# Kernel tuning notes

Measured on AMD Instinct MI355X. Metric: run time of the kernel, lower is better.

## Reference

```python
import jax, jax.numpy as jnp
import numpy as np

B, S, D = 2, 2048, 2048
H = 16
HD = D // H            # 128 head dim
L = 512                # latent dim
R = 64                 # rope dim (min(64, HD) = 64)
RH = R // 2
SCALE = HD ** -0.5     # note: uses head_dim, not head_dim+rope_dim
NEG = jnp.float32(-1e9)


def _rope_tables():
    inv_freq = 1.0 / (10000.0 ** (jnp.arange(0, R, 2, dtype=jnp.float32) / R))  # [RH]
    pos = jnp.arange(S, dtype=jnp.float32)
    freqs = pos[:, None] * inv_freq[None, :]  # [S, RH]
    return jnp.cos(freqs), jnp.sin(freqs)


def _apply_rope(x, cos, sin):
    # x: [B, H, S, R], interleaved even/odd rotation as in the torch source
    xe, xo = x[..., 0::2], x[..., 1::2]                    # [B,H,S,RH]
    c = cos[None, None]
    s = sin[None, None]
    re = xe * c - xo * s
    ro = xe * s + xo * c
    return jnp.stack([re, ro], axis=-1).reshape(x.shape)   # re-interleave


def setup_inputs() -> dict:
    key = jax.random.key(0)
    ks = jax.random.split(key, 8)
    std = 0.02
    f32 = jnp.float32
    return {
        "x":     jax.random.normal(ks[0], (B, S, D), f32),
        "W_ckv": jax.random.normal(ks[1], (D, L), f32) * std,      # compress_kv
        "W_kv":  jax.random.normal(ks[2], (L, 2 * D), f32) * std,  # kv_proj
        "W_cq":  jax.random.normal(ks[3], (D, L), f32) * std,      # compress_q
        "W_q":   jax.random.normal(ks[4], (L, D), f32) * std,      # q_proj
        "W_qr":  jax.random.normal(ks[5], (L, H * R), f32) * std,  # q_rope
        "W_kr":  jax.random.normal(ks[6], (L, R), f32) * std,      # k_rope
        "W_out": jax.random.normal(ks[7], (D, D), f32) * std,      # out_proj
    }


def reference(x, W_ckv, W_kv, W_cq, W_q, W_qr, W_kr, W_out):
    cos, sin = _rope_tables()

    c_kv = x @ W_ckv                                   # [B,S,L]
    kv = c_kv @ W_kv                                   # [B,S,2D]
    c_q = x @ W_cq                                     # [B,S,L]

    q_c = (c_q @ W_q).reshape(B, S, H, HD).transpose(0, 2, 1, 3)    # [B,H,S,HD]
    q_r = (c_q @ W_qr).reshape(B, S, H, R).transpose(0, 2, 1, 3)    # [B,H,S,R]
    k_r = (c_kv @ W_kr)[:, None, :, :]                               # [B,1,S,R]

    k_c, v = jnp.split(kv, 2, axis=-1)
    k_c = k_c.reshape(B, S, H, HD).transpose(0, 2, 1, 3)             # [B,H,S,HD]
    v = v.reshape(B, S, H, HD).transpose(0, 2, 1, 3)                 # [B,H,S,HD]

    q_r = _apply_rope(q_r, cos, sin)
    k_r = jnp.broadcast_to(_apply_rope(k_r, cos, sin), (B, H, S, R))

    q = jnp.concatenate([q_c, q_r], axis=-1)                         # [B,H,S,HD+R]
    k = jnp.concatenate([k_c, k_r], axis=-1)                         # [B,H,S,HD+R]

    scores = jnp.einsum("bhqd,bhkd->bhqk", q, k) * SCALE             # [B,H,S,S]
    causal = jnp.tril(jnp.ones((S, S), dtype=bool))
    scores = jnp.where(causal[None, None], scores, NEG)
    p = jax.nn.softmax(scores, axis=-1)
    attended = jnp.einsum("bhqk,bhkd->bhqd", p, v)                   # [B,H,S,HD]

    out = attended.transpose(0, 2, 1, 3).reshape(B, S, D) @ W_out    # [B,S,D]
    return out  # dropout is identity in eval / p=0
```

## Files before the change

### kernel.cpp

```cpp
#include <hip/hip_runtime.h>
#include <hip/hip_bf16.h>
#include <cstdint>
#include <cstddef>

typedef __bf16 bf16;
typedef __attribute__((ext_vector_type(2))) __bf16 bf16x2;
typedef __attribute__((ext_vector_type(4))) __bf16 bf16x4;
typedef __attribute__((ext_vector_type(8))) __bf16 bf16x8;
typedef __attribute__((ext_vector_type(4))) float f32x4;

#define MFMA16(a, b, c) __builtin_amdgcn_mfma_f32_16x16x32_bf16((a), (b), (c), 0, 0, 0)
#define SCALE_L2E 0.127517432f

#define QCR_STRIDE 3072
#define KV_STRIDE  4160

__device__ __forceinline__ void gload16(const void* g, void* l) {
    __builtin_amdgcn_global_load_lds(
        (const __attribute__((address_space(1))) void*)g,
        (__attribute__((address_space(3))) void*)l, 16, 0, 0);
}

__device__ __forceinline__ void bar_lgkm() {
    asm volatile("s_waitcnt lgkmcnt(0)" ::: "memory");
    __builtin_amdgcn_s_barrier();
    asm volatile("" ::: "memory");
}

__global__ void k_cvt(const float* __restrict__ in, bf16* __restrict__ out, int n4)
{
    int i = blockIdx.x * blockDim.x + threadIdx.x;
    int stride = gridDim.x * blockDim.x;
    const float4* in4 = (const float4*)in;
    bf16x4* o4 = (bf16x4*)out;
    for (; i < n4; i += stride) {
        float4 v = in4[i];
        bf16x4 o;
        o[0] = (bf16)v.x; o[1] = (bf16)v.y; o[2] = (bf16)v.z; o[3] = (bf16)v.w;
        o4[i] = o;
    }
}

__global__ __launch_bounds__(256) void k_cvtT(const float* __restrict__ in,
                                              bf16* __restrict__ out, int Kd, int Nd)
{
    __shared__ float tile[32][33];
    const int k0 = blockIdx.y * 32, n0 = blockIdx.x * 32;
    const int t = threadIdx.x;
    const int r = t >> 3, c4 = (t & 7) * 4;
    float4 v = *(const float4*)(in + (size_t)(k0 + r) * Nd + n0 + c4);
    tile[r][c4 + 0] = v.x; tile[r][c4 + 1] = v.y;
    tile[r][c4 + 2] = v.z; tile[r][c4 + 3] = v.w;
    __syncthreads();
    bf16x4 o;
    o[0] = (bf16)tile[c4 + 0][r]; o[1] = (bf16)tile[c4 + 1][r];
    o[2] = (bf16)tile[c4 + 2][r]; o[3] = (bf16)tile[c4 + 3][r];
    *(bf16x4*)(out + (size_t)(n0 + r) * Kd + k0 + c4) = o;
}

template<int NF, bool F32OUT>
__global__ __launch_bounds__(256) void k_gemm_bt(
    const bf16* __restrict__ A, const bf16* __restrict__ BT,
    bf16* __restrict__ Cb, float* __restrict__ Cf,
    int M, int N, int K, int lda, float cscale)
{
    __shared__ bf16 As[2][4096];
    __shared__ bf16 Bs[2][NF * 1024];

    const int t = threadIdx.x;
    const int m0 = blockIdx.y * 128;
    const int n0 = blockIdx.x * (NF * 32);
    const int wid = t >> 6, lane = t & 63;
    const int wm = (wid >> 1) * 64, wn = (wid & 1) * (NF * 16);
    const int lr = lane & 15, lk = (lane >> 4) * 8;

    const int srow = t >> 2, skc = (t & 3) << 3;
    const int bn0 = min(n0 + srow, N - 1);
    const int bn1 = min(n0 + srow + 64, N - 1);

    f32x4 acc[4][NF];
    const f32x4 z = {0.f, 0.f, 0.f, 0.f};
#pragma unroll
    for (int m = 0; m < 4; ++m)
#pragma unroll
        for (int n = 0; n < NF; ++n) acc[m][n] = z;

    auto stage = [&](int buf, int k0) {
        gload16(BT + (size_t)bn0 * K + k0 + skc, &Bs[buf][t * 8]);
        if constexpr (NF == 4)
            gload16(BT + (size_t)bn1 * K + k0 + skc, &Bs[buf][(t + 256) * 8]);
        gload16(A + (size_t)(m0 + srow) * lda + k0 + skc, &As[buf][t * 8]);
        gload16(A + (size_t)(m0 + srow + 64) * lda + k0 + skc, &As[buf][(t + 256) * 8]);
    };

    stage(0, 0);
    __syncthreads();

    for (int k0 = 0; k0 < K; k0 += 32) {
        const int cur = (k0 >> 5) & 1;
        if (k0 + 32 < K) stage(cur ^ 1, k0 + 32);

        bf16x8 af[4], bfr[NF];
#pragma unroll
        for (int m = 0; m < 4; ++m) af[m] = *(const bf16x8*)(&As[cur][(wm + m * 16 + lr) * 32 + lk]);
#pragma unroll
        for (int n = 0; n < NF; ++n) bfr[n] = *(const bf16x8*)(&Bs[cur][(wn + n * 16 + lr) * 32 + lk]);
#pragma unroll
        for (int m = 0; m < 4; ++m)
#pragma unroll
            for (int n = 0; n < NF; ++n)
                acc[m][n] = MFMA16(af[m], bfr[n], acc[m][n]);

        __syncthreads();
    }

    const int lrow4 = (lane >> 4) * 4;
#pragma unroll
    for (int m = 0; m < 4; ++m)
#pragma unroll
        for (int n = 0; n < NF; ++n)
#pragma unroll
            for (int i = 0; i < 4; ++i) {
                int r = m0 + wm + m * 16 + lrow4 + i;
                int c = n0 + wn + n * 16 + lr;
                if (r < M && c < N) {
                    float val = acc[m][n][i] * cscale;
                    if constexpr (F32OUT) Cf[(size_t)r * N + c] = val;
                    else Cb[(size_t)r * N + c] = (bf16)val;
                }
            }
}

__global__ void k_rope_q(bf16* __restrict__ qcr)
{
    int idx = blockIdx.x * blockDim.x + threadIdx.x;
    int row = idx >> 9;
    int rem = idx & 511;
    int h = rem >> 5;
    int i = rem & 31;
    int s = row & 2047;
    float ang = (float)s * __expf(-(float)i * 0.28782313662f);
    float c = cosf(ang), sn = sinf(ang);
    size_t base = (size_t)row * QCR_STRIDE + 2048 + h * 64 + (i << 1);
    float xe = (float)qcr[base], xo = (float)qcr[base + 1];
    qcr[base] = (bf16)(xe * c - xo * sn);
    qcr[base + 1] = (bf16)(xe * sn + xo * c);
}

__global__ void k_rope_k(bf16* __restrict__ kvkr)
{
    int idx = blockIdx.x * blockDim.x + threadIdx.x;
    int row = idx >> 5;
    int i = idx & 31;
    int s = row & 2047;
    float ang = (float)s * __expf(-(float)i * 0.28782313662f);
    float c = cosf(ang), sn = sinf(ang);
    size_t base = (size_t)row * KV_STRIDE + 4096 + (i << 1);
    float xe = (float)kvkr[base], xo = (float)kvkr[base + 1];
    kvkr[base] = (bf16)(xe * c - xo * sn);
    kvkr[base + 1] = (bf16)(xe * sn + xo * c);
}

__global__ __launch_bounds__(256, 4) void k_attn(
    const bf16* __restrict__ qcr, const bf16* __restrict__ kvkr,
    bf16* __restrict__ att)
{
    __shared__ bf16 Ksc[64 * 128];
    __shared__ bf16 Ksr[64 * 64];
    __shared__ bf16 Vt[128 * 72];
    __shared__ bf16 Pw[4][16 * 72];

    const int L = blockIdx.x;
    const int qt = 31 - (L >> 5);
    const int bh = L & 31;
    const int h = bh & 15, b = bh >> 4;

    const int t = threadIdx.x;
    const int wid = t >> 6, lane = t & 63;
    const int lr = lane & 15, lk = (lane >> 4) * 8, lrow4 = (lane >> 4) * 4;
    const int lq = lane >> 4;
    const size_t rowbase = (size_t)b * 2048;

    const f32x4 z = {0.f, 0.f, 0.f, 0.f};

    const int vk = (t & 31) * 2;
    const int vf = (t >> 5) * 8;

    bf16x8 rc[4], rr[2], rv[4];
    auto LOAD = [&](int kb) {
#pragma unroll
        for (int i = 0; i < 4; ++i) {
            int bb = t + 256 * i;
            int row = bb >> 4, gcb = bb & 15;
            rc[i] = *(const bf16x8*)(kvkr + (rowbase + kb + row) * KV_STRIDE + h * 128 + gcb * 8);
        }
#pragma unroll
        for (int i = 0; i < 2; ++i) {
            int bb = t + 256 * i;
            int row = bb >> 3, gcb = bb & 7;
            rr[i] = *(const bf16x8*)(kvkr + (rowbase + kb + row) * KV_STRIDE + 4096 + gcb * 8);
        }
#pragma unroll
        for (int i = 0; i < 2; ++i) {
            const bf16* vs = kvkr + (rowbase + kb + vk) * KV_STRIDE + 2048 + h * 128 + vf + 64 * i;
            rv[2 * i]     = *(const bf16x8*)vs;
            rv[2 * i + 1] = *(const bf16x8*)(vs + KV_STRIDE);
        }
    };
    auto WRITE = [&]() {
#pragma unroll
        for (int i = 0; i < 4; ++i) {
            int bb = t + 256 * i;
            int row = bb >> 4, gcb = bb & 15;
            int scb = (gcb & 8) | ((gcb ^ row) & 7);
            *(bf16x8*)(Ksc + row * 128 + scb * 8) = rc[i];
        }
#pragma unroll
        for (int i = 0; i < 2; ++i) {
            int bb = t + 256 * i;
            int row = bb >> 3, gcb = bb & 7;
            int scb = (gcb ^ row) & 7;
            *(bf16x8*)(Ksr + row * 64 + scb * 8) = rr[i];
        }
#pragma unroll
        for (int i = 0; i < 2; ++i)
#pragma unroll
            for (int j = 0; j < 8; ++j) {
                bf16x2 pr; pr[0] = rv[2 * i][j]; pr[1] = rv[2 * i + 1][j];
                *(bf16x2*)(Vt + (vf + 64 * i + j) * 72 + vk) = pr;
            }
    };

    const int qrow_w = qt * 64 + wid * 16;

    bf16x8 qf[6];
    {
        const size_t qrow = rowbase + qrow_w + lr;
        const bf16* qp = qcr + qrow * QCR_STRIDE + h * 128;
#pragma unroll
        for (int ks = 0; ks < 4; ++ks) qf[ks] = *(const bf16x8*)(qp + ks * 32 + lk);
        const bf16* qp2 = qcr + qrow * QCR_STRIDE + 2048 + h * 64;
#pragma unroll
        for (int ks = 0; ks < 2; ++ks) qf[4 + ks] = *(const bf16x8*)(qp2 + ks * 32 + lk);
    }

    bf16x8 ones;
#pragma unroll
    for (int j = 0; j < 8; ++j) ones[j] = (bf16)1.0f;

    float mrow[4], lsum[4];
    f32x4 o[8];
#pragma unroll
    for (int i = 0; i < 4; ++i) { mrow[i] = -3e38f; lsum[i] = 0.f; }
#pragma unroll
    for (int n = 0; n < 8; ++n) o[n] = z;

    const int nkt = qt + 1;
    LOAD(0);

#pragma unroll 1
    for (int kt = 0; kt < nkt; ++kt) {
        const int kb = kt * 64;
        bar_lgkm();
        WRITE();
        if (kt + 1 < nkt) LOAD(kb + 64);
        bar_lgkm();

        if (kb > qrow_w + 15) continue;

        f32x4 sacc[4];
#pragma unroll
        for (int kg = 0; kg < 4; ++kg) {
            f32x4 s = z;
            const int key = kg * 16 + lr;
#pragma unroll
            for (int ks = 0; ks < 4; ++ks) {
                int cb = ks * 4 + lq;
                int scb = (cb & 8) | ((cb ^ key) & 7);
                bf16x8 kf = *(const bf16x8*)(Ksc + key * 128 + scb * 8);
                s = MFMA16(qf[ks], kf, s);
            }
#pragma unroll
            for (int ks = 0; ks < 2; ++ks) {
                int cb = ks * 4 + lq;
                int scb = (cb ^ key) & 7;
                bf16x8 kf = *(const bf16x8*)(Ksr + key * 64 + scb * 8);
                s = MFMA16(qf[4 + ks], kf, s);
            }
            sacc[kg] = s;
        }

        const bool domask = (kb + 63) > qrow_w;
        float rmax[4];
#pragma unroll
        for (int i = 0; i < 4; ++i) {
            int qi = qrow_w + lrow4 + i;
            float mx = -3e38f;
#pragma unroll
            for (int kg = 0; kg < 4; ++kg) {
                float v = sacc[kg][i];
                if (domask && (kb + kg * 16 + lr) > qi) v = -3e38f;
                sacc[kg][i] = v;
                mx = fmaxf(mx, v);
            }
            rmax[i] = mx;
        }
#pragma unroll
        for (int d = 1; d < 16; d <<= 1)
#pragma unroll
            for (int i = 0; i < 4; ++i)
                rmax[i] = fmaxf(rmax[i], __shfl_xor(rmax[i], d, 64));

        int anynew = 0;
#pragma unroll
        for (int i = 0; i < 4; ++i)
            if (rmax[i] > mrow[i]) anynew = 1;
        if (__any(anynew)) {
#pragma unroll
            for (int i = 0; i < 4; ++i) {
                float mnew = fmaxf(mrow[i], rmax[i]);
                float scl = __builtin_amdgcn_exp2f(mrow[i] - mnew);
                mrow[i] = mnew;
                lsum[i] *= scl;
#pragma unroll
                for (int n = 0; n < 8; ++n) o[n][i] *= scl;
            }
        }

#pragma unroll
        for (int kg = 0; kg < 4; ++kg)
#pragma unroll
            for (int i = 0; i < 4; ++i)
                sacc[kg][i] = __builtin_amdgcn_exp2f(sacc[kg][i] - mrow[i]);

#pragma unroll
        for (int kg = 0; kg < 4; ++kg)
#pragma unroll
            for (int i = 0; i < 4; ++i)
                Pw[wid][(lrow4 + i) * 72 + kg * 16 + lr] = (bf16)sacc[kg][i];

        f32x4 rs = z;
#pragma unroll
        for (int ks = 0; ks < 2; ++ks) {
            bf16x8 pa = *(const bf16x8*)(&Pw[wid][lr * 72 + ks * 32 + lk]);
            rs = MFMA16(pa, ones, rs);
#pragma unroll
            for (int n = 0; n < 8; ++n) {
                bf16x8 vfr = *(const bf16x8*)(Vt + (n * 16 + lr) * 72 + ks * 32 + lk);
                o[n] = MFMA16(pa, vfr, o[n]);
            }
        }
#pragma unroll
        for (int i = 0; i < 4; ++i) lsum[i] += rs[i];
    }

#pragma unroll
    for (int i = 0; i < 4; ++i) {
        float inv = 1.f / lsum[i];
        size_t orow = (rowbase + qrow_w + lrow4 + i) * 2048 + h * 128;
#pragma unroll
        for (int n = 0; n < 8; ++n)
            att[orow + n * 16 + lr] = (bf16)(o[n][i] * inv);
    }
}

extern "C" void kernel_launch(void* const* d_in, const int* in_sizes, int n_in,
                              void* d_out, int out_size, void* d_ws, size_t ws_size,
                              hipStream_t stream)
{
    (void)in_sizes; (void)n_in; (void)out_size; (void)ws_size;
    const float* x = (const float*)d_in[0];
    const float* w_ckv = (const float*)d_in[1];
    const float* w_kv = (const float*)d_in[2];
    const float* w_cq = (const float*)d_in[3];
    const float* w_q = (const float*)d_in[4];
    const float* w_qr = (const float*)d_in[5];
    const float* w_kr = (const float*)d_in[6];
    const float* w_out = (const float*)d_in[7];
    float* out = (float*)d_out;

    char* ws = (char*)d_ws;
    size_t off = 0;
    auto take = [&](size_t elems) -> bf16* {
        bf16* p = (bf16*)(ws + off);
        off += (elems * sizeof(bf16) + 255) & ~(size_t)255;
        return p;
    };
    bf16* WCT    = take(1024ull * 2048);
    bf16* WKVKRT = take(4160ull * 512);
    bf16* WQQRT  = take(3072ull * 512);
    bf16* C      = take(4096ull * 1024);
    bf16* KVKR   = take(4096ull * 4160);
    bf16* QCR    = take(4096ull * 3072);
    bf16* ATT    = take(4096ull * 2048);
    bf16* WOUTT  = C;
    bf16* XB     = KVKR;

    auto cvtT = [&](const float* in, bf16* o, int K, int N) {
        k_cvtT<<<dim3(N / 32, K / 32), 256, 0, stream>>>(in, o, K, N);
    };
    cvtT(w_ckv, WCT, 2048, 512);
    cvtT(w_cq, WCT + 512ull * 2048, 2048, 512);
    cvtT(w_kv, WKVKRT, 512, 4096);
    cvtT(w_kr, WKVKRT + 4096ull * 512, 512, 64);
    cvtT(w_q, WQQRT, 512, 2048);
    cvtT(w_qr, WQQRT + 2048ull * 512, 512, 1024);

    k_cvt<<<2048, 256, 0, stream>>>(x, XB, (4096 * 2048) / 4);

    k_gemm_bt<2, false><<<dim3(16, 32), 256, 0, stream>>>(
        XB, WCT, C, nullptr, 4096, 1024, 2048, 2048, 1.0f);
    k_gemm_bt<4, false><<<dim3(33, 32), 256, 0, stream>>>(
        C, WKVKRT, KVKR, nullptr, 4096, 4160, 512, 1024, 1.0f);
    k_gemm_bt<4, false><<<dim3(24, 32), 256, 0, stream>>>(
        C + 512, WQQRT, QCR, nullptr, 4096, 3072, 512, 1024, SCALE_L2E);

    cvtT(w_out, WOUTT, 2048, 2048);

    k_rope_q<<<8192, 256, 0, stream>>>(QCR);
    k_rope_k<<<512, 256, 0, stream>>>(KVKR);

    k_attn<<<1024, 256, 0, stream>>>(QCR, KVKR, ATT);

    k_gemm_bt<4, true><<<dim3(16, 32), 256, 0, stream>>>(
        ATT, WOUTT, nullptr, out, 4096, 2048, 2048, 2048, 1.0f);
}
```

Baseline: 294.7 us.

## Keep attention probabilities in registers via transposed MFMA and merge weight-transpose launches

The attention kernel swaps MFMA operand order to compute S^T, so each lane holds one query row. Row max and row sum become lane-local plus two cross-lane shuffles, and P is packed straight into registers as the B operand for the PV MFMA. This removes the per-wave LDS round trip for P, the ones-vector MFMA used for row sums, and the 16-lane max reduction. K rows are permuted on write and V is stored in a swizzled 64-wide layout instead of a padded one; launch bounds drop from 4 to 3 waves per SIMD, which allows more registers at the cost of occupancy. Separately, the six weight transpose launches are merged into a single kernel to cut launch overhead.

```diff
diff --git a/kernel.cpp b/kernel.cpp
--- a/kernel.cpp
+++ b/kernel.cpp
@@ -25,6 +25,11 @@
     asm volatile("s_waitcnt lgkmcnt(0)" ::: "memory");
     __builtin_amdgcn_s_barrier();
     asm volatile("" ::: "memory");
+}
+
+__device__ __forceinline__ int pack_bf16(float a, float b) {
+    bf16x2 p; p[0] = (bf16)a; p[1] = (bf16)b;
+    return __builtin_bit_cast(int, p);
 }
 
 __global__ void k_cvt(const float* __restrict__ in, bf16* __restrict__ out, int n4)
@@ -58,6 +63,35 @@
     *(bf16x4*)(out + (size_t)(n0 + r) * Kd + k0 + c4) = o;
 }
 
+__global__ __launch_bounds__(256) void k_cvtT6(
+    const float* __restrict__ w_ckv, const float* __restrict__ w_kv,
+    const float* __restrict__ w_cq, const float* __restrict__ w_q,
+    const float* __restrict__ w_qr, const float* __restrict__ w_kr,
+    bf16* __restrict__ WCT, bf16* __restrict__ WKVKRT, bf16* __restrict__ WQQRT)
+{
+    __shared__ float tile[32][33];
+    int bid = blockIdx.x;
+    const float* src; bf16* dst; int Kd, Nd, loc;
+    if (bid < 1024)      { src = w_ckv; dst = WCT;                   Kd = 2048; Nd = 512;  loc = bid; }
+    else if (bid < 3072) { src = w_kv;  dst = WKVKRT;                Kd = 512;  Nd = 4096; loc = bid - 1024; }
+    else if (bid < 4096) { src = w_cq;  dst = WCT + 512ull * 2048;   Kd = 2048; Nd = 512;  loc = bid - 3072; }
+    else if (bid < 5120) { src = w_q;   dst = WQQRT;                 Kd = 512;  Nd = 2048; loc = bid - 4096; }
+    else if (bid < 5632) { src = w_qr;  dst = WQQRT + 2048ull * 512; Kd = 512;  Nd = 1024; loc = bid - 5120; }
+    else                 { src = w_kr;  dst = WKVKRT + 4096ull * 512; Kd = 512; Nd = 64;   loc = bid - 5632; }
+    const int nbx = Nd / 32;
+    const int n0 = (loc % nbx) * 32, k0 = (loc / nbx) * 32;
+    const int t = threadIdx.x;
+    const int r = t >> 3, c4 = (t & 7) * 4;
+    float4 v = *(const float4*)(src + (size_t)(k0 + r) * Nd + n0 + c4);
+    tile[r][c4 + 0] = v.x; tile[r][c4 + 1] = v.y;
+    tile[r][c4 + 2] = v.z; tile[r][c4 + 3] = v.w;
+    __syncthreads();
+    bf16x4 o;
+    o[0] = (bf16)tile[c4 + 0][r]; o[1] = (bf16)tile[c4 + 1][r];
+    o[2] = (bf16)tile[c4 + 2][r]; o[3] = (bf16)tile[c4 + 3][r];
+    *(bf16x4*)(dst + (size_t)(n0 + r) * Kd + k0 + c4) = o;
+}
+
 template<int NF, bool F32OUT>
 __global__ __launch_bounds__(256) void k_gemm_bt(
     const bf16* __restrict__ A, const bf16* __restrict__ BT,
@@ -161,14 +195,13 @@
     kvkr[base + 1] = (bf16)(xe * sn + xo * c);
 }
 
-__global__ __launch_bounds__(256, 4) void k_attn(
+__global__ __launch_bounds__(256, 3) void k_attn(
     const bf16* __restrict__ qcr, const bf16* __restrict__ kvkr,
     bf16* __restrict__ att)
 {
     __shared__ bf16 Ksc[64 * 128];
     __shared__ bf16 Ksr[64 * 64];
-    __shared__ bf16 Vt[128 * 72];
-    __shared__ bf16 Pw[4][16 * 72];
+    __shared__ bf16 Vt[128 * 64];
 
     const int L = blockIdx.x;
     const int qt = 31 - (L >> 5);
@@ -177,11 +210,14 @@
 
     const int t = threadIdx.x;
     const int wid = t >> 6, lane = t & 63;
-    const int lr = lane & 15, lk = (lane >> 4) * 8, lrow4 = (lane >> 4) * 4;
-    const int lq = lane >> 4;
+    const int lr = lane & 15, lq = lane >> 4, lk = lq * 8;
     const size_t rowbase = (size_t)b * 2048;
 
     const f32x4 z = {0.f, 0.f, 0.f, 0.f};
+
+    auto rho = [](int r) {
+        return (((r >> 5) & 1) << 5) | (((r >> 2) & 1) << 4) | (((r >> 3) & 3) << 2) | (r & 3);
+    };
 
     const int vk = (t & 31) * 2;
     const int vf = (t >> 5) * 8;
@@ -211,14 +247,14 @@
 #pragma unroll
         for (int i = 0; i < 4; ++i) {
             int bb = t + 256 * i;
-            int row = bb >> 4, gcb = bb & 15;
+            int row = rho(bb >> 4), gcb = bb & 15;
             int scb = (gcb & 8) | ((gcb ^ row) & 7);
             *(bf16x8*)(Ksc + row * 128 + scb * 8) = rc[i];
         }
 #pragma unroll
         for (int i = 0; i < 2; ++i) {
             int bb = t + 256 * i;
-            int row = bb >> 3, gcb = bb & 7;
+            int row = rho(bb >> 3), gcb = bb & 7;
             int scb = (gcb ^ row) & 7;
             *(bf16x8*)(Ksr + row * 64 + scb * 8) = rr[i];
         }
@@ -226,16 +262,19 @@
         for (int i = 0; i < 2; ++i)
 #pragma unroll
             for (int j = 0; j < 8; ++j) {
+                int feat = vf + 64 * i + j;
+                int scb = ((vk >> 3) ^ (feat & 7)) & 7;
                 bf16x2 pr; pr[0] = rv[2 * i][j]; pr[1] = rv[2 * i + 1][j];
-                *(bf16x2*)(Vt + (vf + 64 * i + j) * 72 + vk) = pr;
+                *(bf16x2*)(Vt + feat * 64 + scb * 8 + (vk & 7)) = pr;
             }
     };
 
     const int qrow_w = qt * 64 + wid * 16;
+    const int qi = qrow_w + lr;
 
     bf16x8 qf[6];
     {
-        const size_t qrow = rowbase + qrow_w + lr;
+        const size_t qrow = rowbase + qi;
         const bf16* qp = qcr + qrow * QCR_STRIDE + h * 128;
 #pragma unroll
         for (int ks = 0; ks < 4; ++ks) qf[ks] = *(const bf16x8*)(qp + ks * 32 + lk);
@@ -244,14 +283,8 @@
         for (int ks = 0; ks < 2; ++ks) qf[4 + ks] = *(const bf16x8*)(qp2 + ks * 32 + lk);
     }
 
-    bf16x8 ones;
-#pragma unroll
-    for (int j = 0; j < 8; ++j) ones[j] = (bf16)1.0f;
-
-    float mrow[4], lsum[4];
+    float mrow = -3e38f, lsum = 0.f;
     f32x4 o[8];
-#pragma unroll
-    for (int i = 0; i < 4; ++i) { mrow[i] = -3e38f; lsum[i] = 0.f; }
 #pragma unroll
     for (int n = 0; n < 8; ++n) o[n] = z;
 
@@ -278,89 +311,87 @@
                 int cb = ks * 4 + lq;
                 int scb = (cb & 8) | ((cb ^ key) & 7);
                 bf16x8 kf = *(const bf16x8*)(Ksc + key * 128 + scb * 8);
-                s = MFMA16(qf[ks], kf, s);
+                s = MFMA16(kf, qf[ks], s);
             }
 #pragma unroll
             for (int ks = 0; ks < 2; ++ks) {
                 int cb = ks * 4 + lq;
                 int scb = (cb ^ key) & 7;
                 bf16x8 kf = *(const bf16x8*)(Ksr + key * 64 + scb * 8);
-                s = MFMA16(qf[4 + ks], kf, s);
+                s = MFMA16(kf, qf[4 + ks], s);
             }
             sacc[kg] = s;
         }
 
         const bool domask = (kb + 63) > qrow_w;
-        float rmax[4];
-#pragma unroll
-        for (int i = 0; i < 4; ++i) {
-            int qi = qrow_w + lrow4 + i;
-            float mx = -3e38f;
+        if (domask) {
 #pragma unroll
             for (int kg = 0; kg < 4; ++kg) {
-                float v = sacc[kg][i];
-                if (domask && (kb + kg * 16 + lr) > qi) v = -3e38f;
-                sacc[kg][i] = v;
-                mx = fmaxf(mx, v);
-            }
-            rmax[i] = mx;
-        }
-#pragma unroll
-        for (int d = 1; d < 16; d <<= 1)
-#pragma unroll
-            for (int i = 0; i < 4; ++i)
-                rmax[i] = fmaxf(rmax[i], __shfl_xor(rmax[i], d, 64));
-
-        int anynew = 0;
+                int keybase = kb + ((kg >> 1) << 5) + (lq << 3) + ((kg & 1) << 2);
+#pragma unroll
+                for (int i = 0; i < 4; ++i)
+                    if (keybase + i > qi) sacc[kg][i] = -3e38f;
+            }
+        }
+
+        f32x4 mv;
 #pragma unroll
         for (int i = 0; i < 4; ++i)
-            if (rmax[i] > mrow[i]) anynew = 1;
-        if (__any(anynew)) {
+            mv[i] = fmaxf(fmaxf(sacc[0][i], sacc[1][i]), fmaxf(sacc[2][i], sacc[3][i]));
+        float mx = fmaxf(fmaxf(mv[0], mv[1]), fmaxf(mv[2], mv[3]));
+        mx = fmaxf(mx, __shfl_xor(mx, 16, 64));
+        mx = fmaxf(mx, __shfl_xor(mx, 32, 64));
+
+        if (__any(mx > mrow)) {
+            float mnew = fmaxf(mrow, mx);
+            float scl = __builtin_amdgcn_exp2f(mrow - mnew);
+            mrow = mnew;
+            lsum *= scl;
+#pragma unroll
+            for (int n = 0; n < 8; ++n)
+#pragma unroll
+                for (int i = 0; i < 4; ++i) o[n][i] *= scl;
+        }
+
+        f32x4 sv = z;
+#pragma unroll
+        for (int kg = 0; kg < 4; ++kg)
 #pragma unroll
             for (int i = 0; i < 4; ++i) {
-                float mnew = fmaxf(mrow[i], rmax[i]);
-                float scl = __builtin_amdgcn_exp2f(mrow[i] - mnew);
-                mrow[i] = mnew;
-                lsum[i] *= scl;
-#pragma unroll
-                for (int n = 0; n < 8; ++n) o[n][i] *= scl;
-            }
-        }
-
-#pragma unroll
-        for (int kg = 0; kg < 4; ++kg)
-#pragma unroll
-            for (int i = 0; i < 4; ++i)
-                sacc[kg][i] = __builtin_amdgcn_exp2f(sacc[kg][i] - mrow[i]);
-
-#pragma unroll
-        for (int kg = 0; kg < 4; ++kg)
-#pragma unroll
-            for (int i = 0; i < 4; ++i)
-                Pw[wid][(lrow4 + i) * 72 + kg * 16 + lr] = (bf16)sacc[kg][i];
-
-        f32x4 rs = z;
-#pragma unroll
-        for (int ks = 0; ks < 2; ++ks) {
-            bf16x8 pa = *(const bf16x8*)(&Pw[wid][lr * 72 + ks * 32 + lk]);
-            rs = MFMA16(pa, ones, rs);
+                float pv = __builtin_amdgcn_exp2f(sacc[kg][i] - mrow);
+                sacc[kg][i] = pv;
+                sv[i] += pv;
+            }
+        float rs = (sv[0] + sv[1]) + (sv[2] + sv[3]);
+        rs += __shfl_xor(rs, 16, 64);
+        rs += __shfl_xor(rs, 32, 64);
+        lsum += rs;
+
+#pragma unroll
+        for (int s = 0; s < 2; ++s) {
+            union { int4 iv; bf16x8 v; } pb;
+            pb.iv.x = pack_bf16(sacc[2 * s][0], sacc[2 * s][1]);
+            pb.iv.y = pack_bf16(sacc[2 * s][2], sacc[2 * s][3]);
+            pb.iv.z = pack_bf16(sacc[2 * s + 1][0], sacc[2 * s + 1][1]);
+            pb.iv.w = pack_bf16(sacc[2 * s + 1][2], sacc[2 * s + 1][3]);
 #pragma unroll
             for (int n = 0; n < 8; ++n) {
-                bf16x8 vfr = *(const bf16x8*)(Vt + (n * 16 + lr) * 72 + ks * 32 + lk);
-                o[n] = MFMA16(pa, vfr, o[n]);
-            }
-        }
-#pragma unroll
-        for (int i = 0; i < 4; ++i) lsum[i] += rs[i];
+                int feat = n * 16 + lr;
+                int scb = ((s * 4 + lq) ^ (feat & 7)) & 7;
+                bf16x8 vfr = *(const bf16x8*)(Vt + feat * 64 + scb * 8);
+                o[n] = MFMA16(vfr, pb.v, o[n]);
+            }
+        }
     }
 
-#pragma unroll
-    for (int i = 0; i < 4; ++i) {
-        float inv = 1.f / lsum[i];
-        size_t orow = (rowbase + qrow_w + lrow4 + i) * 2048 + h * 128;
-#pragma unroll
-        for (int n = 0; n < 8; ++n)
-            att[orow + n * 16 + lr] = (bf16)(o[n][i] * inv);
+    const float inv = 1.f / lsum;
+    const size_t orow = (rowbase + qi) * 2048 + h * 128;
+#pragma unroll
+    for (int n = 0; n < 8; ++n) {
+        bf16x4 ov;
+#pragma unroll
+        for (int i = 0; i < 4; ++i) ov[i] = (bf16)(o[n][i] * inv);
+        *(bf16x4*)(att + orow + n * 16 + (lq << 2)) = ov;
     }
 }
 
@@ -396,15 +427,8 @@
     bf16* WOUTT  = C;
     bf16* XB     = KVKR;
 
-    auto cvtT = [&](const float* in, bf16* o, int K, int N) {
-        k_cvtT<<<dim3(N / 32, K / 32), 256, 0, stream>>>(in, o, K, N);
-    };
-    cvtT(w_ckv, WCT, 2048, 512);
-    cvtT(w_cq, WCT + 512ull * 2048, 2048, 512);
-    cvtT(w_kv, WKVKRT, 512, 4096);
-    cvtT(w_kr, WKVKRT + 4096ull * 512, 512, 64);
-    cvtT(w_q, WQQRT, 512, 2048);
-    cvtT(w_qr, WQQRT + 2048ull * 512, 512, 1024);
+    k_cvtT6<<<5664, 256, 0, stream>>>(w_ckv, w_kv, w_cq, w_q, w_qr, w_kr,
+                                      WCT, WKVKRT, WQQRT);
 
     k_cvt<<<2048, 256, 0, stream>>>(x, XB, (4096 * 2048) / 4);
 
@@ -415,7 +439,7 @@
     k_gemm_bt<4, false><<<dim3(24, 32), 256, 0, stream>>>(
         C + 512, WQQRT, QCR, nullptr, 4096, 3072, 512, 1024, SCALE_L2E);
 
-    cvtT(w_out, WOUTT, 2048, 2048);
+    k_cvtT<<<dim3(64, 64), 256, 0, stream>>>(w_out, WOUTT, 2048, 2048);
 
     k_rope_q<<<8192, 256, 0, stream>>>(QCR);
     k_rope_k<<<512, 256, 0, stream>>>(KVKR);
```

New measurement: 261.1 us. 1.13x faster.
